# Optimization experiments

Hardware: AMD Instinct MI355X
Metric: run time of the kernel (lower is better)

Reference implementation:

```python
import jax, jax.numpy as jnp
import numpy as np
from jax.scipy.special import gammaln

EPS = 1e-20
EULER_GAMMA = 0.5772156649015329
B, L, D, H, DK, DV = 8, 512, 1024, 16, 64, 64
K_WEIBULL = 0.5
BETA_GAMMA = 1.0
SCALE = 1.0 / np.sqrt(DK)  # torch code DIVIDES by this -> multiply by sqrt(DK)


def setup_inputs() -> dict:
    key = jax.random.key(0)
    ks = jax.random.split(key, 20)
    f = jnp.float32
    return {
        "queries": jax.random.normal(ks[0], (B, L, D), f),
        "keys": jax.random.normal(ks[1], (B, L, D), f),
        "values": jax.random.normal(ks[2], (B, L, D), f),
        "unif": jax.random.uniform(ks[3], (B, H, L, L), f),
        "Wq": jax.random.normal(ks[4], (D, H * DK), f) * 0.03,
        "bq": jnp.zeros((H * DK,), f),
        "Wk": jax.random.normal(ks[5], (D, H * DK), f) * 0.03,
        "bk": jnp.zeros((H * DK,), f),
        "Wv": jax.random.normal(ks[6], (D, H * DV), f) * 0.03,
        "bv": jnp.zeros((H * DV,), f),
        "Wo": jax.random.normal(ks[7], (H * DV, D), f) * 0.03,
        "bo": jnp.zeros((D,), f),
        "Wp1": jax.random.normal(ks[8], (DK, D), f) * 0.05,
        "bp1": jnp.zeros((D,), f),
        "Wp2": jax.random.normal(ks[9], (D, 1), f) * 0.05,
        "bp2": jnp.zeros((1,), f),
    }


def reference(queries, keys, values, unif, Wq, bq, Wk, bk, Wv, bv, Wo, bo, Wp1, bp1, Wp2, bp2):
    # projections -> multi-head layout
    q = (queries @ Wq + bq).reshape(B, L, H, DK).transpose(0, 2, 1, 3)   # [B,H,Q,dk]
    k = (keys @ Wk + bk).reshape(B, L, H, DK).transpose(0, 2, 1, 3)     # [B,H,K,dk]
    v = (values @ Wv + bv).reshape(B, L, H, DV).transpose(0, 2, 1, 3)   # [B,H,K,dv]

    # faithful: torch divides by scale=1/sqrt(dk)
    att = jnp.einsum("bhqd,bhkd->bhqk", q, k) / SCALE                   # [B,H,Q,K]

    # prior MLP on keys (per key position)
    h = (k @ Wp1 + bp1)                                                  # [B,H,K,D]
    h = jnp.where(h >= 0, h, 0.01 * h)                                   # LeakyReLU
    dot_gamma = (h @ Wp2 + bp2).transpose(0, 1, 3, 2)                    # [B,H,1,K]
    prior_w = jax.nn.softmax(dot_gamma, axis=-1)
    alpha = prior_w * BETA_GAMMA                                         # [B,H,1,K]

    # Weibull reparameterized stochastic attention
    inv_k = 1.0 / K_WEIBULL
    logprobs = jnp.log(jax.nn.softmax(att, axis=-1) + EPS)
    gumbel_w = jnp.log(-jnp.log(1.0 - unif + EPS) + EPS)
    att_s = jax.nn.softmax(logprobs - gammaln(1.0 + inv_k + inv_k * gumbel_w), axis=-1)

    lg1 = gammaln(jnp.float32(1.0 + inv_k))
    kl = -(alpha * (logprobs - lg1)
           - EULER_GAMMA * alpha * inv_k
           - BETA_GAMMA * jnp.exp(logprobs - lg1 + lg1)
           + alpha * jnp.log(BETA_GAMMA + EPS)
           - gammaln(alpha + EPS))
    kl_mean = kl.mean()

    out = jnp.einsum("bhqk,bhkd->bhqd", att_s, v)                        # [B,H,Q,dv]
    out = out.transpose(0, 2, 1, 3).reshape(B, L, H * DV)
    out = out @ Wo + bo                                                  # [B,Q,D]
    return out, kl_mean
```

## Files before the change

### kernel.cpp

```cpp
#include <hip/hip_runtime.h>
#include <math.h>


typedef __bf16 bh_t;
typedef bh_t  bh8  __attribute__((ext_vector_type(8)));
typedef float f32x4 __attribute__((ext_vector_type(4)));
typedef _Float16 hf_t;
typedef hf_t  hf4  __attribute__((ext_vector_type(4)));

#define MFMA_BF16 __builtin_amdgcn_mfma_f32_16x16x32_bf16

static constexpr size_t PE = 4096ull*1024ull;
static constexpr size_t P2 = PE*2ull;
static constexpr size_t W2 = 1024ull*1024ull*2ull;
static constexpr size_t O_QHI = 0;
static constexpr size_t O_QLO = O_QHI + P2;
static constexpr size_t O_KHI = O_QLO + P2;
static constexpr size_t O_KLO = O_KHI + P2;
static constexpr size_t O_VT  = O_KLO + P2;
static constexpr size_t O_WQH = O_VT  + P2;
static constexpr size_t O_WQL = O_WQH + W2;
static constexpr size_t O_WKH = O_WQL + W2;
static constexpr size_t O_WKL = O_WKH + W2;
static constexpr size_t O_WVH = O_WKL + W2;
static constexpr size_t O_WVL = O_WVH + W2;
static constexpr size_t O_WOH = O_WVL + W2;
static constexpr size_t O_WOL = O_WOH + W2;
static constexpr size_t O_WP1H = O_WOL + W2;
static constexpr size_t O_WP1L = O_WP1H + 1024ull*64ull*2ull;
static constexpr size_t O_DG   = O_WP1L + 1024ull*64ull*2ull;
static constexpr size_t O_ALPHA= O_DG + 65536ull*4ull;
static constexpr size_t O_HO   = O_ALPHA + 65536ull*4ull;
static constexpr size_t O_GS   = O_HO + P2;
static constexpr size_t O_ACC  = O_GS + 512ull*65536ull*2ull;
static constexpr size_t O_AQH  = O_ACC + 256;
static constexpr size_t WS_TOTAL = O_AQH + 5ull*P2;

__device__ __align__(256) unsigned char g_ws[WS_TOTAL];

__device__ __forceinline__ float lgamma_fast(float x)
{
    float ax = (x < 0.5f) ? (1.0f - x) : x;
    float p  = ax*(ax+1.f)*(ax+2.f)*(ax+3.f);
    bool  sm = ax < 4.0f;
    float lsh = sm ? __logf(p) : 0.0f;
    float y   = sm ? (ax + 4.0f) : ax;
    float ly  = __logf(y);
    float inv = __builtin_amdgcn_rcpf(y);
    float i2  = inv * inv;
    float stir = fmaf(y - 0.5f, ly, -y) + 0.91893853320467274f
               + inv * fmaf(-2.7777777777e-3f, i2, 8.3333333333e-2f);
    float core = stir - lsh;
    float r  = x - rintf(x);
    float sp = __sinf(3.14159265358979f * r);
    float rres = 1.14472988584940017f - __logf(fabsf(sp)) - core;
    return (x < 0.5f) ? rres : core;
}

__global__ __launch_bounds__(256) void k_transpose_split(
    const float* __restrict__ in, bh_t* __restrict__ oh, bh_t* __restrict__ ol,
    int rows, int cols)
{
    __shared__ float tile[64][65];
    const int bc = blockIdx.x * 64, br = blockIdx.y * 64;
    const int t = threadIdx.x;
    const int r = t >> 2, c0 = (t & 3) * 16;
#pragma unroll
    for (int i = 0; i < 16; i += 4) {
        float4 v = *(const float4*)(in + (size_t)(br + r) * cols + bc + c0 + i);
        tile[r][c0+i]   = v.x; tile[r][c0+i+1] = v.y;
        tile[r][c0+i+2] = v.z; tile[r][c0+i+3] = v.w;
    }
    __syncthreads();
    bh8 hv[2], lv[2];
#pragma unroll
    for (int i = 0; i < 16; i++) {
        float x = tile[c0 + i][r];
        bh_t hh = (bh_t)x;
        hv[i >> 3][i & 7] = hh;
        lv[i >> 3][i & 7] = (bh_t)(x - (float)hh);
    }
    size_t ob = (size_t)(bc + r) * rows + br + c0;
    *(bh8*)(oh + ob)     = hv[0];
    *(bh8*)(oh + ob + 8) = hv[1];
    *(bh8*)(ol + ob)     = lv[0];
    *(bh8*)(ol + ob + 8) = lv[1];
}

__global__ __launch_bounds__(256) void k_transpose_split4(
    const float* __restrict__ W0, const float* __restrict__ W1,
    const float* __restrict__ W2_, const float* __restrict__ W3,
    bh_t* __restrict__ OH, double* __restrict__ acc)
{
    __shared__ float tile[64][65];
    const int z = blockIdx.z;
    if (z == 0 && blockIdx.x == 0 && blockIdx.y == 0 && threadIdx.x < 4)
        acc[threadIdx.x] = 0.0;
    const float* in = (z == 0) ? W0 : (z == 1) ? W1 : (z == 2) ? W2_ : W3;
    bh_t* oh = OH + (size_t)z * 2ull * 1024ull * 1024ull;
    bh_t* ol = oh + 1024ull * 1024ull;
    const int bc = blockIdx.x * 64, br = blockIdx.y * 64;
    const int t = threadIdx.x;
    const int r = t >> 2, c0 = (t & 3) * 16;
#pragma unroll
    for (int i = 0; i < 16; i += 4) {
        float4 v = *(const float4*)(in + (size_t)(br + r) * 1024 + bc + c0 + i);
        tile[r][c0+i]   = v.x; tile[r][c0+i+1] = v.y;
        tile[r][c0+i+2] = v.z; tile[r][c0+i+3] = v.w;
    }
    __syncthreads();
    bh8 hv[2], lv[2];
#pragma unroll
    for (int i = 0; i < 16; i++) {
        float x = tile[c0 + i][r];
        bh_t hh = (bh_t)x;
        hv[i >> 3][i & 7] = hh;
        lv[i >> 3][i & 7] = (bh_t)(x - (float)hh);
    }
    size_t ob = (size_t)(bc + r) * 1024 + br + c0;
    *(bh8*)(oh + ob)     = hv[0];
    *(bh8*)(oh + ob + 8) = hv[1];
    *(bh8*)(ol + ob)     = lv[0];
    *(bh8*)(ol + ob + 8) = lv[1];
}

__global__ __launch_bounds__(256) void k_splitA(
    const float* __restrict__ q, const float* __restrict__ k,
    const float* __restrict__ v, bh_t* __restrict__ dst)
{
    const int z = blockIdx.y;
    const float* in = (z == 0) ? q : (z == 1) ? k : v;
    size_t idx = ((size_t)blockIdx.x * 256 + threadIdx.x) * 8;
    float4 v0 = *(const float4*)(in + idx);
    float4 v1 = *(const float4*)(in + idx + 4);
    float xs[8] = {v0.x, v0.y, v0.z, v0.w, v1.x, v1.y, v1.z, v1.w};
    bh8 h, l;
#pragma unroll
    for (int i = 0; i < 8; i++) {
        bh_t hh = (bh_t)xs[i];
        h[i] = hh;
        l[i] = (bh_t)(xs[i] - (float)hh);
    }
    if (z < 2) {
        bh_t* hp = dst + (size_t)z * 2 * PE;
        *(bh8*)(hp + idx)      = h;
        *(bh8*)(hp + PE + idx) = l;
    } else {
        *(bh8*)(dst + 4 * PE + idx) = h;
    }
}

template<bool SPLIT, int OMODE>
__device__ __forceinline__ void gemm_body(
    const bh_t* __restrict__ ABH, const bh_t* __restrict__ ABL,
    const bh_t* __restrict__ WH, const bh_t* __restrict__ WL,
    const float* __restrict__ bias,
    bh_t* __restrict__ oh, bh_t* __restrict__ ol, float* __restrict__ of,
    int n0, int m0)
{
    __shared__ __align__(16) bh_t Ah[128][40];
    __shared__ __align__(16) bh_t Al[128][40];
    __shared__ __align__(16) bh_t Bh[128][40];
    __shared__ __align__(16) bh_t Bl[128][40];
    const int t = threadIdx.x;
    const int lane = t & 63, w = t >> 6;
    const int lr = lane & 15, kg = lane >> 4;
    const int wm = (w & 1) * 64, wn = (w >> 1) * 64;
    const int ar = t >> 2, ac = (t & 3) * 8;
    f32x4 acc[4][4] = {};

    for (int kt = 0; kt < 1024; kt += 32) {
        __syncthreads();
        {
            size_t a0 = (size_t)(m0 + ar) * 1024 + kt + ac;
            size_t a1 = (size_t)(m0 + ar + 64) * 1024 + kt + ac;
            *(bh8*)&Ah[ar][ac]      = *(const bh8*)(ABH + a0);
            *(bh8*)&Ah[ar + 64][ac] = *(const bh8*)(ABH + a1);
            if constexpr (SPLIT) {
                *(bh8*)&Al[ar][ac]      = *(const bh8*)(ABL + a0);
                *(bh8*)&Al[ar + 64][ac] = *(const bh8*)(ABL + a1);
            }
            size_t b0 = (size_t)(n0 + ar) * 1024 + kt + ac;
            size_t b1 = (size_t)(n0 + ar + 64) * 1024 + kt + ac;
            *(bh8*)&Bh[ar][ac]      = *(const bh8*)(WH + b0);
            *(bh8*)&Bh[ar + 64][ac] = *(const bh8*)(WH + b1);
            if constexpr (SPLIT) {
                *(bh8*)&Bl[ar][ac]      = *(const bh8*)(WL + b0);
                *(bh8*)&Bl[ar + 64][ac] = *(const bh8*)(WL + b1);
            }
        }
        __syncthreads();
        bh8 bfh[4], bfl[4];
#pragma unroll
        for (int fn = 0; fn < 4; fn++) {
            bfh[fn] = *(bh8*)&Bh[wn + fn*16 + lr][kg * 8];
            if constexpr (SPLIT) bfl[fn] = *(bh8*)&Bl[wn + fn*16 + lr][kg * 8];
        }
#pragma unroll
        for (int fm = 0; fm < 4; fm++) {
            bh8 a_h = *(bh8*)&Ah[wm + fm*16 + lr][kg * 8];
            bh8 a_l;
            if constexpr (SPLIT) a_l = *(bh8*)&Al[wm + fm*16 + lr][kg * 8];
#pragma unroll
            for (int fn = 0; fn < 4; fn++) {
                acc[fm][fn] = MFMA_BF16(a_h, bfh[fn], acc[fm][fn], 0, 0, 0);
                if constexpr (SPLIT) {
                    acc[fm][fn] = MFMA_BF16(a_h, bfl[fn], acc[fm][fn], 0, 0, 0);
                    acc[fm][fn] = MFMA_BF16(a_l, bfh[fn], acc[fm][fn], 0, 0, 0);
                }
            }
        }
    }
#pragma unroll
    for (int fm = 0; fm < 4; fm++)
#pragma unroll
    for (int fn = 0; fn < 4; fn++) {
        int col = n0 + wn + fn*16 + lr;
        float bv = bias[col];
#pragma unroll
        for (int r = 0; r < 4; r++) {
            int row = m0 + wm + fm*16 + kg*4 + r;
            float c = acc[fm][fn][r] + bv;
            size_t idx = (size_t)row * 1024 + col;
            if constexpr (OMODE == 0) {
                bh_t hh = (bh_t)c;
                oh[idx] = hh;
                ol[idx] = (bh_t)(c - (float)hh);
            } else if constexpr (OMODE == 1) {
                oh[idx] = (bh_t)c;
            } else if constexpr (OMODE == 2) {
                of[idx] = c;
            } else {
                int bb = row >> 9, ll = row & 511;
                oh[(((size_t)(bb*16 + (col >> 6)) * 64) + (col & 63)) * 512 + ll] = (bh_t)c;
            }
        }
    }
}

template<int OMODE>
__global__ __launch_bounds__(256) void k_gemm(
    const bh_t* __restrict__ ABH,
    const bh_t* __restrict__ WH, const bh_t* __restrict__ WL,
    const float* __restrict__ bias,
    bh_t* __restrict__ oh, float* __restrict__ of,
    const double* __restrict__ acc)
{
    gemm_body<false, OMODE>(ABH, nullptr, WH, WL, bias, oh, nullptr, of,
                            blockIdx.x * 128, blockIdx.y * 128);
    if constexpr (OMODE == 2) {
        if (blockIdx.x == 0 && blockIdx.y == 0 && threadIdx.x == 0) {
            double kl = (-acc[0] + 512.0 * acc[2] + 65536.0) / 33554432.0;
            of[4194304] = (float)kl;
        }
    }
}

__global__ __launch_bounds__(256) void k_gemm_qk(
    const bh_t* __restrict__ Abase, const bh_t* __restrict__ Wbase,
    const float* __restrict__ bq, const float* __restrict__ bk,
    bh_t* __restrict__ Obase)
{
    const int z = blockIdx.z;
    const bh_t* AH = Abase + (size_t)z * 2 * PE;
    const bh_t* WH = Wbase + (size_t)z * 2ull * 1024ull * 1024ull;
    bh_t* oh = Obase + (size_t)z * 2 * PE;
    gemm_body<true, 0>(AH, AH + PE, WH, WH + 1024ull*1024ull,
                       z ? bk : bq, oh, oh + PE, nullptr,
                       blockIdx.x * 128, blockIdx.y * 128);
}

__global__ __launch_bounds__(256) void k_prior(
    const bh_t* __restrict__ KH, const bh_t* __restrict__ WP1T,
    const float* __restrict__ bp1, const float* __restrict__ wp2,
    const float* __restrict__ bp2, float* __restrict__ DG)
{
    __shared__ __align__(16) bh_t Kt[64][72];
    __shared__ __align__(16) bh_t Wt[64][72];
    const int lt = blockIdx.x, h = blockIdx.y, b = blockIdx.z;
    const int t = threadIdx.x, lane = t & 63, w = t >> 6;
    const int lr = lane & 15, kg = lane >> 4;
    {
        int r = t >> 2, j0 = (t & 3) * 16;
        const bh_t* src = KH + ((size_t)(b*512 + lt*64 + r)) * 1024 + h*64 + j0;
        *(bh8*)&Kt[r][j0]     = *(const bh8*)src;
        *(bh8*)&Kt[r][j0 + 8] = *(const bh8*)(src + 8);
    }
    __syncthreads();
    bh8 af0 = *(bh8*)&Kt[w*16 + lr][kg * 8];
    bh8 af1 = *(bh8*)&Kt[w*16 + lr][32 + kg * 8];
    float dgp[4] = {0.f, 0.f, 0.f, 0.f};
    for (int dt = 0; dt < 16; dt++) {
        __syncthreads();
        {
            int r = t >> 2, j0 = (t & 3) * 16;
            const bh_t* src = WP1T + (size_t)(dt*64 + r) * 64 + j0;
            *(bh8*)&Wt[r][j0]     = *(const bh8*)src;
            *(bh8*)&Wt[r][j0 + 8] = *(const bh8*)(src + 8);
        }
        __syncthreads();
#pragma unroll
        for (int fn = 0; fn < 4; fn++) {
            bh8 b0 = *(bh8*)&Wt[fn*16 + lr][kg * 8];
            bh8 b1 = *(bh8*)&Wt[fn*16 + lr][32 + kg * 8];
            f32x4 acc = {};
            acc = MFMA_BF16(af0, b0, acc, 0, 0, 0);
            acc = MFMA_BF16(af1, b1, acc, 0, 0, 0);
            int d = dt*64 + fn*16 + lr;
            float bpv = bp1[d], wvv = wp2[d];
#pragma unroll
            for (int r = 0; r < 4; r++) {
                float hv = acc[r] + bpv;
                hv = (hv >= 0.f) ? hv : 0.01f * hv;
                dgp[r] = fmaf(hv, wvv, dgp[r]);
            }
        }
    }
#pragma unroll
    for (int r = 0; r < 4; r++) {
        float v = dgp[r];
        v += __shfl_xor(v, 1); v += __shfl_xor(v, 2);
        v += __shfl_xor(v, 4); v += __shfl_xor(v, 8);
        dgp[r] = v;
    }
    if (lr == 0) {
        float b2 = bp2[0];
        int bh = b * 16 + h;
#pragma unroll
        for (int r = 0; r < 4; r++)
            DG[(size_t)bh*512 + lt*64 + w*16 + kg*4 + r] = dgp[r] + b2;
    }
}

__global__ __launch_bounds__(512) void k_alpha(
    const float* __restrict__ DG, float* __restrict__ AL, double* __restrict__ acc)
{
    __shared__ float red[512];
    const int bh = blockIdx.x, t = threadIdx.x;
    float v = DG[(size_t)bh * 512 + t];
    red[t] = v; __syncthreads();
    for (int s = 256; s > 0; s >>= 1) { if (t < s) red[t] = fmaxf(red[t], red[t+s]); __syncthreads(); }
    float m = red[0]; __syncthreads();
    float e = expf(v - m);
    red[t] = e; __syncthreads();
    for (int s = 256; s > 0; s >>= 1) { if (t < s) red[t] += red[t+s]; __syncthreads(); }
    float ssum = red[0]; __syncthreads();
    float a = e / ssum;
    AL[(size_t)bh * 512 + t] = a;
    float t2 = a * 1.8475785103630112f + lgammaf(a + 1e-20f);
    red[t] = t2; __syncthreads();
    for (int s = 256; s > 0; s >>= 1) { if (t < s) red[t] += red[t+s]; __syncthreads(); }
    if (t == 0) atomicAdd(&acc[2], (double)red[0]);
}

__global__ __launch_bounds__(512, 3) void k_attn(
    const bh_t* __restrict__ QH, const bh_t* __restrict__ QL,
    const bh_t* __restrict__ KH, const bh_t* __restrict__ KL,
    const bh_t* __restrict__ VT, const float* __restrict__ U,
    const float* __restrict__ AL, bh_t* __restrict__ HOB,
    hf_t* __restrict__ GS, double* __restrict__ acc)
{
    __shared__ __align__(16) bh_t KtH[64][72];
    __shared__ __align__(16) bh_t KtL[64][72];
    __shared__ __align__(16) bh_t Vt[64][72];
    __shared__ __align__(16) bh_t Sl[8][16][72];
    __shared__ float Asm[64];
    __shared__ float red[512];

    const int flat = blockIdx.x;
    const int bh = flat & 127, qc = flat >> 7;
    const int b = bh >> 4, h = bh & 15;
    const int t = threadIdx.x, w = t >> 6, lane = t & 63;
    const int lr = lane & 15, kg = lane >> 4;
    const int q0 = qc * 128 + w * 16;
    const int sr = t >> 3, sj = (t & 7) * 8;
    const float* Up = U + ((size_t)bh * 512 + q0 + kg * 4) * 512;
    hf_t* GSp = GS + (size_t)flat * 65536 + (size_t)w * 8192;

    bh8 qh[2], ql[2];
    {
        size_t qb = ((size_t)(b * 512) + q0 + lr) * 1024 + h * 64;
        qh[0] = *(const bh8*)(QH + qb + kg * 8);
        qh[1] = *(const bh8*)(QH + qb + 32 + kg * 8);
        ql[0] = *(const bh8*)(QL + qb + kg * 8);
        ql[1] = *(const bh8*)(QL + qb + 32 + kg * 8);
    }
    float C[4];

    {
        float M1[4], Z1[4];
#pragma unroll
        for (int r = 0; r < 4; r++) { M1[r] = -INFINITY; Z1[r] = 0.f; }

        for (int kt = 0; kt < 8; kt++) {
            __syncthreads();
            {
                size_t src = ((size_t)(b*512 + kt*64 + sr)) * 1024 + h*64 + sj;
                *(bh8*)&KtH[sr][sj] = *(const bh8*)(KH + src);
                *(bh8*)&KtL[sr][sj] = *(const bh8*)(KL + src);
            }
            __syncthreads();
            f32x4 av[4];
#pragma unroll
            for (int fn = 0; fn < 4; fn++) {
                f32x4 a = {};
#pragma unroll
                for (int ks = 0; ks < 2; ks++) {
                    bh8 kb  = *(bh8*)&KtH[fn*16 + lr][ks*32 + kg*8];
                    bh8 kl2 = *(bh8*)&KtL[fn*16 + lr][ks*32 + kg*8];
                    a = MFMA_BF16(qh[ks], kb,  a, 0, 0, 0);
                    a = MFMA_BF16(qh[ks], kl2, a, 0, 0, 0);
                    a = MFMA_BF16(ql[ks], kb,  a, 0, 0, 0);
                }
#pragma unroll
                for (int r = 0; r < 4; r++) a[r] *= 8.0f;
                av[fn] = a;
                int k = kt * 64 + fn * 16 + lr;
                hf4 gh;
#pragma unroll
                for (int r = 0; r < 4; r++) {
                    float u  = Up[(size_t)r * 512 + k];
                    float tt = (1.0f - u) + 1e-20f;
                    float gl = 1e-20f - __logf(tt);
                    float g  = __logf(gl);
                    gh[r] = (hf_t)lgamma_fast(fmaf(2.0f, g, 3.0f));
                }
                *(hf4*)(GSp + ((size_t)(kt*4 + fn) * 64 + lane) * 4) = gh;
            }
#pragma unroll
            for (int r = 0; r < 4; r++) {
                float mx = fmaxf(fmaxf(av[0][r], av[1][r]), fmaxf(av[2][r], av[3][r]));
                mx = fmaxf(mx, __shfl_xor(mx, 1));
                mx = fmaxf(mx, __shfl_xor(mx, 2));
                mx = fmaxf(mx, __shfl_xor(mx, 4));
                mx = fmaxf(mx, __shfl_xor(mx, 8));
                float nm = fmaxf(M1[r], mx);
                float es = __expf(av[0][r]-nm) + __expf(av[1][r]-nm)
                         + __expf(av[2][r]-nm) + __expf(av[3][r]-nm);
                es += __shfl_xor(es, 1); es += __shfl_xor(es, 2);
                es += __shfl_xor(es, 4); es += __shfl_xor(es, 8);
                Z1[r] = Z1[r] * __expf(M1[r] - nm) + es;
                M1[r] = nm;
            }
        }
#pragma unroll
        for (int r = 0; r < 4; r++) C[r] = M1[r] + logf(Z1[r]);
    }

    float M2[4], Z2[4];
    f32x4 oacc[4] = {};
#pragma unroll
    for (int r = 0; r < 4; r++) { M2[r] = -INFINITY; Z2[r] = 0.f; }
    float S1f = 0.f;

    for (int kt = 0; kt < 8; kt++) {
        __syncthreads();
        {
            size_t src = ((size_t)(b*512 + kt*64 + sr)) * 1024 + h*64 + sj;
            *(bh8*)&KtH[sr][sj] = *(const bh8*)(KH + src);
            *(bh8*)&KtL[sr][sj] = *(const bh8*)(KL + src);
            const bh_t* vsrc = VT + ((size_t)bh * 64 + sr) * 512 + kt*64 + sj;
            *(bh8*)&Vt[sr][sj] = *(const bh8*)vsrc;
            if (t < 64) Asm[t] = AL[(size_t)bh * 512 + kt * 64 + t];
        }
        __syncthreads();
        f32x4 wv[4];
#pragma unroll
        for (int fn = 0; fn < 4; fn++) {
            f32x4 a = {};
#pragma unroll
            for (int ks = 0; ks < 2; ks++) {
                bh8 kb  = *(bh8*)&KtH[fn*16 + lr][ks*32 + kg*8];
                bh8 kl2 = *(bh8*)&KtL[fn*16 + lr][ks*32 + kg*8];
                a = MFMA_BF16(qh[ks], kb,  a, 0, 0, 0);
                a = MFMA_BF16(qh[ks], kl2, a, 0, 0, 0);
                a = MFMA_BF16(ql[ks], kb,  a, 0, 0, 0);
            }
            hf4 gh = *(const hf4*)(GSp + ((size_t)(kt*4 + fn) * 64 + lane) * 4);
            float alv = Asm[fn * 16 + lr];
#pragma unroll
            for (int r = 0; r < 4; r++) {
                float s  = fmaf(a[r], 8.0f, -C[r]);
                float ex = __expf(s);
                float lp = __logf(ex + 1e-20f);
                wv[fn][r] = lp - (float)gh[r];
                S1f = fmaf(alv, lp, S1f);
            }
        }
#pragma unroll
        for (int r = 0; r < 4; r++) {
            float mx = fmaxf(fmaxf(wv[0][r], wv[1][r]), fmaxf(wv[2][r], wv[3][r]));
            mx = fmaxf(mx, __shfl_xor(mx, 1));
            mx = fmaxf(mx, __shfl_xor(mx, 2));
            mx = fmaxf(mx, __shfl_xor(mx, 4));
            mx = fmaxf(mx, __shfl_xor(mx, 8));
            float nm = fmaxf(M2[r], mx);
            float sc = __expf(M2[r] - nm);
            float zs = 0.f;
#pragma unroll
            for (int fn = 0; fn < 4; fn++) {
                float sv = __expf(wv[fn][r] - nm);
                zs += sv;
                Sl[w][kg * 4 + r][fn * 16 + lr] = (bh_t)sv;
            }
            zs += __shfl_xor(zs, 1); zs += __shfl_xor(zs, 2);
            zs += __shfl_xor(zs, 4); zs += __shfl_xor(zs, 8);
            Z2[r] = fmaf(Z2[r], sc, zs);
            M2[r] = nm;
#pragma unroll
            for (int fo = 0; fo < 4; fo++) oacc[fo][r] *= sc;
        }
        bh8 sa0 = *(bh8*)&Sl[w][lr][kg*8];
        bh8 sa1 = *(bh8*)&Sl[w][lr][32 + kg*8];
#pragma unroll
        for (int fo = 0; fo < 4; fo++) {
            bh8 v0 = *(bh8*)&Vt[fo*16 + lr][kg*8];
            bh8 v1 = *(bh8*)&Vt[fo*16 + lr][32 + kg*8];
            oacc[fo] = MFMA_BF16(sa0, v0, oacc[fo], 0, 0, 0);
            oacc[fo] = MFMA_BF16(sa1, v1, oacc[fo], 0, 0, 0);
        }
    }
    float rz[4];
#pragma unroll
    for (int r = 0; r < 4; r++) rz[r] = 1.0f / Z2[r];
#pragma unroll
    for (int fo = 0; fo < 4; fo++) {
#pragma unroll
        for (int r = 0; r < 4; r++) {
            int q = q0 + kg * 4 + r;
            int dv = fo * 16 + lr;
            HOB[((size_t)(b * 512 + q)) * 1024 + h * 64 + dv] = (bh_t)(oacc[fo][r] * rz[r]);
        }
    }
    red[t] = S1f; __syncthreads();
    for (int s = 256; s > 0; s >>= 1) { if (t < s) red[t] += red[t+s]; __syncthreads(); }
    if (t == 0) atomicAdd(&acc[0], (double)red[0]);
}

extern "C" void kernel_launch(void* const* d_in, const int* in_sizes, int n_in,
                              void* d_out, int out_size, void* d_ws, size_t ws_size,
                              hipStream_t stream)
{
    (void)in_sizes; (void)n_in; (void)d_ws; (void)ws_size; (void)out_size;
    const float* queries = (const float*)d_in[0];
    const float* keys    = (const float*)d_in[1];
    const float* values  = (const float*)d_in[2];
    const float* unif    = (const float*)d_in[3];
    const float* Wq = (const float*)d_in[4];  const float* bq = (const float*)d_in[5];
    const float* Wk = (const float*)d_in[6];  const float* bk = (const float*)d_in[7];
    const float* Wv = (const float*)d_in[8];  const float* bv = (const float*)d_in[9];
    const float* Wo = (const float*)d_in[10]; const float* bo = (const float*)d_in[11];
    const float* Wp1 = (const float*)d_in[12]; const float* bp1 = (const float*)d_in[13];
    const float* Wp2 = (const float*)d_in[14]; const float* bp2 = (const float*)d_in[15];

    unsigned char* ws = nullptr;
    hipGetSymbolAddress((void**)&ws, HIP_SYMBOL(g_ws));

    bh_t* QHI = (bh_t*)(ws + O_QHI); bh_t* QLO = (bh_t*)(ws + O_QLO);
    bh_t* KHI = (bh_t*)(ws + O_KHI); bh_t* KLO = (bh_t*)(ws + O_KLO);
    bh_t* VTp = (bh_t*)(ws + O_VT);
    bh_t* WQH = (bh_t*)(ws + O_WQH);
    bh_t* WVH = (bh_t*)(ws + O_WVH); bh_t* WVL = (bh_t*)(ws + O_WVL);
    bh_t* WOH = (bh_t*)(ws + O_WOH); bh_t* WOL = (bh_t*)(ws + O_WOL);
    bh_t* WP1H = (bh_t*)(ws + O_WP1H); bh_t* WP1L = (bh_t*)(ws + O_WP1L);
    float* DG    = (float*)(ws + O_DG);
    float* ALPHA = (float*)(ws + O_ALPHA);
    bh_t*  HOB   = (bh_t*)(ws + O_HO);
    hf_t*  GS    = (hf_t*)(ws + O_GS);
    double* ACC  = (double*)(ws + O_ACC);
    bh_t*  AQH   = (bh_t*)(ws + O_AQH);
    bh_t*  AVH   = AQH + 4 * PE;
    float* outF  = (float*)d_out;

    k_transpose_split4<<<dim3(16,16,4), 256, 0, stream>>>(Wq, Wk, Wv, Wo, WQH, ACC);
    k_transpose_split<<<dim3(16,1), 256, 0, stream>>>(Wp1, WP1H, WP1L, 64, 1024);
    k_splitA<<<dim3(2048,3), 256, 0, stream>>>(queries, keys, values, AQH);

    k_gemm_qk<<<dim3(8,32,2), 256, 0, stream>>>(AQH, WQH, bq, bk, QHI);
    k_gemm<3><<<dim3(8,32), 256, 0, stream>>>(AVH, WVH, WVL, bv, VTp, nullptr, nullptr);

    k_prior<<<dim3(8,16,8), 256, 0, stream>>>(KHI, WP1H, bp1, Wp2, bp2, DG);
    k_alpha<<<128, 512, 0, stream>>>(DG, ALPHA, ACC);

    k_attn<<<512, 512, 0, stream>>>(QHI, QLO, KHI, KLO, VTp, unif, ALPHA, HOB, GS, ACC);

    k_gemm<2><<<dim3(8,32), 256, 0, stream>>>(HOB, WOH, WOL, bo, nullptr, outF, ACC);
}
```

Before: 339.7 us.

## Split attention over key halves with separate stats, merge, and combine kernels

Splits the fused two-pass attention kernel into a key-split first pass (partial max/sum), a small merge kernel for the log-normalizer, a key-split second pass writing unnormalized partial outputs plus stats, and a combine kernel that rescales and writes the bf16 head output. This doubles the grid from 512 to 1024 blocks and raises the occupancy hint so more waves keep the MI355X busy. It also rewrites lgamma_fast to use fewer logs and replaces log(exp(s)+eps) with a max-plus-correction form. The cost is two extra launches and extra global traffic for the partial outputs and stats.

```diff
diff --git a/kernel.cpp b/kernel.cpp
--- a/kernel.cpp
+++ b/kernel.cpp
@@ -34,27 +34,29 @@
 static constexpr size_t O_GS   = O_HO + P2;
 static constexpr size_t O_ACC  = O_GS + 512ull*65536ull*2ull;
 static constexpr size_t O_AQH  = O_ACC + 256;
-static constexpr size_t WS_TOTAL = O_AQH + 5ull*P2;
+static constexpr size_t O_PS   = O_AQH + 5ull*P2;
+static constexpr size_t O_CB   = O_PS + 1024ull*128ull*2ull*4ull;
+static constexpr size_t O_MZ   = O_CB + 512ull*128ull*4ull;
+static constexpr size_t O_OP   = O_MZ + 1024ull*128ull*2ull*4ull;
+static constexpr size_t WS_TOTAL = O_OP + 1024ull*128ull*64ull*4ull;
 
 __device__ __align__(256) unsigned char g_ws[WS_TOTAL];
 
 __device__ __forceinline__ float lgamma_fast(float x)
 {
     float ax = (x < 0.5f) ? (1.0f - x) : x;
-    float p  = ax*(ax+1.f)*(ax+2.f)*(ax+3.f);
     bool  sm = ax < 4.0f;
-    float lsh = sm ? __logf(p) : 0.0f;
-    float y   = sm ? (ax + 4.0f) : ax;
-    float ly  = __logf(y);
-    float inv = __builtin_amdgcn_rcpf(y);
-    float i2  = inv * inv;
-    float stir = fmaf(y - 0.5f, ly, -y) + 0.91893853320467274f
-               + inv * fmaf(-2.7777777777e-3f, i2, 8.3333333333e-2f);
-    float core = stir - lsh;
+    float p  = sm ? ax*(ax+1.f)*(ax+2.f)*(ax+3.f) : 1.0f;
+    float y  = sm ? (ax + 4.0f) : ax;
+    float ly = __logf(y);
+    float stir = fmaf(y - 0.5f, ly, -y) + 0.91893853320467274f;
     float r  = x - rintf(x);
     float sp = __sinf(3.14159265358979f * r);
-    float rres = 1.14472988584940017f - __logf(fabsf(sp)) - core;
-    return (x < 0.5f) ? rres : core;
+    bool  rf = x < 0.5f;
+    float rarg = rf ? fabsf(sp) : p;
+    float rnum = rf ? p : 1.0f;
+    float lA = __logf(rnum * __builtin_amdgcn_rcpf(rarg));
+    return (rf ? (1.14472988584940017f - stir) : stir) + lA;
 }
 
 __global__ __launch_bounds__(256) void k_transpose_split(
@@ -353,21 +355,17 @@
     if (t == 0) atomicAdd(&acc[2], (double)red[0]);
 }
 
-__global__ __launch_bounds__(512, 3) void k_attn(
+__global__ __launch_bounds__(512, 8) void k_attnA(
     const bh_t* __restrict__ QH, const bh_t* __restrict__ QL,
     const bh_t* __restrict__ KH, const bh_t* __restrict__ KL,
-    const bh_t* __restrict__ VT, const float* __restrict__ U,
-    const float* __restrict__ AL, bh_t* __restrict__ HOB,
-    hf_t* __restrict__ GS, double* __restrict__ acc)
+    const float* __restrict__ U, hf_t* __restrict__ GS,
+    float* __restrict__ PS)
 {
     __shared__ __align__(16) bh_t KtH[64][72];
     __shared__ __align__(16) bh_t KtL[64][72];
-    __shared__ __align__(16) bh_t Vt[64][72];
-    __shared__ __align__(16) bh_t Sl[8][16][72];
-    __shared__ float Asm[64];
-    __shared__ float red[512];
-
-    const int flat = blockIdx.x;
+
+    const int bid = blockIdx.x;
+    const int split = bid >> 9, flat = bid & 511;
     const int bh = flat & 127, qc = flat >> 7;
     const int b = bh >> 4, h = bh & 15;
     const int t = threadIdx.x, w = t >> 6, lane = t & 63;
@@ -385,75 +383,128 @@
         ql[0] = *(const bh8*)(QL + qb + kg * 8);
         ql[1] = *(const bh8*)(QL + qb + 32 + kg * 8);
     }
-    float C[4];
-
+    float M1[4], Z1[4];
+#pragma unroll
+    for (int r = 0; r < 4; r++) { M1[r] = -INFINITY; Z1[r] = 0.f; }
+
+    for (int kt = split * 4; kt < split * 4 + 4; kt++) {
+        __syncthreads();
+        {
+            size_t src = ((size_t)(b*512 + kt*64 + sr)) * 1024 + h*64 + sj;
+            *(bh8*)&KtH[sr][sj] = *(const bh8*)(KH + src);
+            *(bh8*)&KtL[sr][sj] = *(const bh8*)(KL + src);
+        }
+        __syncthreads();
+        f32x4 av[4];
+#pragma unroll
+        for (int fn = 0; fn < 4; fn++) {
+            f32x4 a = {};
+#pragma unroll
+            for (int ks = 0; ks < 2; ks++) {
+                bh8 kb  = *(bh8*)&KtH[fn*16 + lr][ks*32 + kg*8];
+                bh8 kl2 = *(bh8*)&KtL[fn*16 + lr][ks*32 + kg*8];
+                a = MFMA_BF16(qh[ks], kb,  a, 0, 0, 0);
+                a = MFMA_BF16(qh[ks], kl2, a, 0, 0, 0);
+                a = MFMA_BF16(ql[ks], kb,  a, 0, 0, 0);
+            }
+#pragma unroll
+            for (int r = 0; r < 4; r++) a[r] *= 8.0f;
+            av[fn] = a;
+            int k = kt * 64 + fn * 16 + lr;
+            hf4 gh;
+#pragma unroll
+            for (int r = 0; r < 4; r++) {
+                float u  = Up[(size_t)r * 512 + k];
+                float tt = (1.0f - u) + 1e-20f;
+                float gl = 1e-20f - __logf(tt);
+                float g  = __logf(gl);
+                gh[r] = (hf_t)lgamma_fast(fmaf(2.0f, g, 3.0f));
+            }
+            *(hf4*)(GSp + ((size_t)(kt*4 + fn) * 64 + lane) * 4) = gh;
+        }
+#pragma unroll
+        for (int r = 0; r < 4; r++) {
+            float mx = fmaxf(fmaxf(av[0][r], av[1][r]), fmaxf(av[2][r], av[3][r]));
+            mx = fmaxf(mx, __shfl_xor(mx, 1));
+            mx = fmaxf(mx, __shfl_xor(mx, 2));
+            mx = fmaxf(mx, __shfl_xor(mx, 4));
+            mx = fmaxf(mx, __shfl_xor(mx, 8));
+            float nm = fmaxf(M1[r], mx);
+            float es = __expf(av[0][r]-nm) + __expf(av[1][r]-nm)
+                     + __expf(av[2][r]-nm) + __expf(av[3][r]-nm);
+            es += __shfl_xor(es, 1); es += __shfl_xor(es, 2);
+            es += __shfl_xor(es, 4); es += __shfl_xor(es, 8);
+            Z1[r] = Z1[r] * __expf(M1[r] - nm) + es;
+            M1[r] = nm;
+        }
+    }
+    if (lr == 0) {
+#pragma unroll
+        for (int r = 0; r < 4; r++) {
+            size_t row = (size_t)bid * 128 + (w*16 + kg*4 + r);
+            PS[row * 2]     = M1[r];
+            PS[row * 2 + 1] = Z1[r];
+        }
+    }
+}
+
+__global__ __launch_bounds__(512) void k_mergeC(
+    const float* __restrict__ PS, float* __restrict__ CB)
+{
+    int idx = blockIdx.x * 512 + threadIdx.x;
+    float Ma = PS[(size_t)idx * 2],           Za = PS[(size_t)idx * 2 + 1];
+    float Mb = PS[(size_t)(65536 + idx) * 2], Zb = PS[(size_t)(65536 + idx) * 2 + 1];
+    float M = fmaxf(Ma, Mb);
+    float Z = Za * __expf(Ma - M) + Zb * __expf(Mb - M);
+    CB[idx] = M + __logf(Z);
+}
+
+__global__ __launch_bounds__(512, 6) void k_attnB(
+    const bh_t* __restrict__ QH, const bh_t* __restrict__ QL,
+    const bh_t* __restrict__ KH, const bh_t* __restrict__ KL,
+    const bh_t* __restrict__ VT, const float* __restrict__ AL,
+    const hf_t* __restrict__ GS, const float* __restrict__ CB,
+    float* __restrict__ OP, float* __restrict__ MZ,
+    double* __restrict__ acc)
+{
+    __shared__ __align__(16) bh_t KtH[64][72];
+    __shared__ __align__(16) bh_t KtL[64][72];
+    __shared__ __align__(16) bh_t Vt[64][72];
+    __shared__ __align__(16) bh_t Sl[8][16][72];
+    __shared__ float Asm[64];
+    __shared__ float red[512];
+
+    const int bid = blockIdx.x;
+    const int split = bid >> 9, flat = bid & 511;
+    const int bh = flat & 127, qc = flat >> 7;
+    const int b = bh >> 4, h = bh & 15;
+    const int t = threadIdx.x, w = t >> 6, lane = t & 63;
+    const int lr = lane & 15, kg = lane >> 4;
+    const int q0 = qc * 128 + w * 16;
+    const int sr = t >> 3, sj = (t & 7) * 8;
+    const hf_t* GSp = GS + (size_t)flat * 65536 + (size_t)w * 8192;
+
+    bh8 qh[2], ql[2];
     {
-        float M1[4], Z1[4];
-#pragma unroll
-        for (int r = 0; r < 4; r++) { M1[r] = -INFINITY; Z1[r] = 0.f; }
-
-        for (int kt = 0; kt < 8; kt++) {
-            __syncthreads();
-            {
-                size_t src = ((size_t)(b*512 + kt*64 + sr)) * 1024 + h*64 + sj;
-                *(bh8*)&KtH[sr][sj] = *(const bh8*)(KH + src);
-                *(bh8*)&KtL[sr][sj] = *(const bh8*)(KL + src);
-            }
-            __syncthreads();
-            f32x4 av[4];
-#pragma unroll
-            for (int fn = 0; fn < 4; fn++) {
-                f32x4 a = {};
-#pragma unroll
-                for (int ks = 0; ks < 2; ks++) {
-                    bh8 kb  = *(bh8*)&KtH[fn*16 + lr][ks*32 + kg*8];
-                    bh8 kl2 = *(bh8*)&KtL[fn*16 + lr][ks*32 + kg*8];
-                    a = MFMA_BF16(qh[ks], kb,  a, 0, 0, 0);
-                    a = MFMA_BF16(qh[ks], kl2, a, 0, 0, 0);
-                    a = MFMA_BF16(ql[ks], kb,  a, 0, 0, 0);
-                }
-#pragma unroll
-                for (int r = 0; r < 4; r++) a[r] *= 8.0f;
-                av[fn] = a;
-                int k = kt * 64 + fn * 16 + lr;
-                hf4 gh;
-#pragma unroll
-                for (int r = 0; r < 4; r++) {
-                    float u  = Up[(size_t)r * 512 + k];
-                    float tt = (1.0f - u) + 1e-20f;
-                    float gl = 1e-20f - __logf(tt);
-                    float g  = __logf(gl);
-                    gh[r] = (hf_t)lgamma_fast(fmaf(2.0f, g, 3.0f));
-                }
-                *(hf4*)(GSp + ((size_t)(kt*4 + fn) * 64 + lane) * 4) = gh;
-            }
-#pragma unroll
-            for (int r = 0; r < 4; r++) {
-                float mx = fmaxf(fmaxf(av[0][r], av[1][r]), fmaxf(av[2][r], av[3][r]));
-                mx = fmaxf(mx, __shfl_xor(mx, 1));
-                mx = fmaxf(mx, __shfl_xor(mx, 2));
-                mx = fmaxf(mx, __shfl_xor(mx, 4));
-                mx = fmaxf(mx, __shfl_xor(mx, 8));
-                float nm = fmaxf(M1[r], mx);
-                float es = __expf(av[0][r]-nm) + __expf(av[1][r]-nm)
-                         + __expf(av[2][r]-nm) + __expf(av[3][r]-nm);
-                es += __shfl_xor(es, 1); es += __shfl_xor(es, 2);
-                es += __shfl_xor(es, 4); es += __shfl_xor(es, 8);
-                Z1[r] = Z1[r] * __expf(M1[r] - nm) + es;
-                M1[r] = nm;
-            }
-        }
-#pragma unroll
-        for (int r = 0; r < 4; r++) C[r] = M1[r] + logf(Z1[r]);
-    }
+        size_t qb = ((size_t)(b * 512) + q0 + lr) * 1024 + h * 64;
+        qh[0] = *(const bh8*)(QH + qb + kg * 8);
+        qh[1] = *(const bh8*)(QH + qb + 32 + kg * 8);
+        ql[0] = *(const bh8*)(QL + qb + kg * 8);
+        ql[1] = *(const bh8*)(QL + qb + 32 + kg * 8);
+    }
+    float C4[4];
+#pragma unroll
+    for (int r = 0; r < 4; r++)
+        C4[r] = CB[flat * 128 + w*16 + kg*4 + r];
 
     float M2[4], Z2[4];
     f32x4 oacc[4] = {};
 #pragma unroll
     for (int r = 0; r < 4; r++) { M2[r] = -INFINITY; Z2[r] = 0.f; }
     float S1f = 0.f;
-
-    for (int kt = 0; kt < 8; kt++) {
+    const float LEPS = 46.0517019f;
+
+    for (int kt = split * 4; kt < split * 4 + 4; kt++) {
         __syncthreads();
         {
             size_t src = ((size_t)(b*512 + kt*64 + sr)) * 1024 + h*64 + sj;
@@ -464,7 +515,7 @@
             if (t < 64) Asm[t] = AL[(size_t)bh * 512 + kt * 64 + t];
         }
         __syncthreads();
-        f32x4 wv[4];
+        f32x4 wv[4], zq[4];
 #pragma unroll
         for (int fn = 0; fn < 4; fn++) {
             f32x4 a = {};
@@ -480,11 +531,13 @@
             float alv = Asm[fn * 16 + lr];
 #pragma unroll
             for (int r = 0; r < 4; r++) {
-                float s  = fmaf(a[r], 8.0f, -C[r]);
-                float ex = __expf(s);
-                float lp = __logf(ex + 1e-20f);
-                wv[fn][r] = lp - (float)gh[r];
-                S1f = fmaf(alv, lp, S1f);
+                float s  = fmaf(a[r], 8.0f, -C4[r]);
+                float m0 = fmaxf(s, -LEPS);
+                float d  = fabsf(s + LEPS);
+                float z  = __expf(-d);
+                zq[fn][r] = z;
+                S1f = fmaf(alv, m0 + z * fmaf(-0.5f, z, 1.0f), S1f);
+                wv[fn][r] = m0 - (float)gh[r];
             }
         }
 #pragma unroll
@@ -494,12 +547,12 @@
             mx = fmaxf(mx, __shfl_xor(mx, 2));
             mx = fmaxf(mx, __shfl_xor(mx, 4));
             mx = fmaxf(mx, __shfl_xor(mx, 8));
-            float nm = fmaxf(M2[r], mx);
+            float nm = fmaxf(M2[r], mx + 0.6931472f);
             float sc = __expf(M2[r] - nm);
             float zs = 0.f;
 #pragma unroll
             for (int fn = 0; fn < 4; fn++) {
-                float sv = __expf(wv[fn][r] - nm);
+                float sv = __expf(wv[fn][r] - nm) * (1.0f + zq[fn][r]);
                 zs += sv;
                 Sl[w][kg * 4 + r][fn * 16 + lr] = (bh_t)sv;
             }
@@ -520,21 +573,46 @@
             oacc[fo] = MFMA_BF16(sa1, v1, oacc[fo], 0, 0, 0);
         }
     }
-    float rz[4];
-#pragma unroll
-    for (int r = 0; r < 4; r++) rz[r] = 1.0f / Z2[r];
 #pragma unroll
     for (int fo = 0; fo < 4; fo++) {
 #pragma unroll
         for (int r = 0; r < 4; r++) {
-            int q = q0 + kg * 4 + r;
-            int dv = fo * 16 + lr;
-            HOB[((size_t)(b * 512 + q)) * 1024 + h * 64 + dv] = (bh_t)(oacc[fo][r] * rz[r]);
+            size_t row = (size_t)bid * 128 + (w*16 + kg*4 + r);
+            OP[row * 64 + (fo*16 + lr)] = oacc[fo][r];
+        }
+    }
+    if (lr == 0) {
+#pragma unroll
+        for (int r = 0; r < 4; r++) {
+            size_t row = (size_t)bid * 128 + (w*16 + kg*4 + r);
+            MZ[row * 2]     = M2[r];
+            MZ[row * 2 + 1] = Z2[r];
         }
     }
     red[t] = S1f; __syncthreads();
     for (int s = 256; s > 0; s >>= 1) { if (t < s) red[t] += red[t+s]; __syncthreads(); }
     if (t == 0) atomicAdd(&acc[0], (double)red[0]);
+}
+
+__global__ __launch_bounds__(256) void k_comb(
+    const float* __restrict__ OP, const float* __restrict__ MZ,
+    bh_t* __restrict__ HOB)
+{
+    size_t idx = (size_t)blockIdx.x * 256 + threadIdx.x;
+    int dv = idx & 63;
+    int rowg = (int)(idx >> 6);
+    float Ma = MZ[(size_t)rowg * 2],             Za = MZ[(size_t)rowg * 2 + 1];
+    float Mb = MZ[(size_t)(65536 + rowg) * 2],   Zb = MZ[(size_t)(65536 + rowg) * 2 + 1];
+    float M  = fmaxf(Ma, Mb);
+    float wa = __expf(Ma - M), wb = __expf(Mb - M);
+    float Z  = Za * wa + Zb * wb;
+    float o  = OP[(size_t)rowg * 64 + dv] * wa
+             + OP[(size_t)(65536 + rowg) * 64 + dv] * wb;
+    int flat = rowg >> 7, rl = rowg & 127;
+    int bh = flat & 127, qc = flat >> 7;
+    int b = bh >> 4, h = bh & 15;
+    int q = qc * 128 + rl;
+    HOB[((size_t)(b * 512 + q)) * 1024 + h * 64 + dv] = (bh_t)(o / Z);
 }
 
 extern "C" void kernel_launch(void* const* d_in, const int* in_sizes, int n_in,
@@ -570,6 +648,10 @@
     double* ACC  = (double*)(ws + O_ACC);
     bh_t*  AQH   = (bh_t*)(ws + O_AQH);
     bh_t*  AVH   = AQH + 4 * PE;
+    float* PS    = (float*)(ws + O_PS);
+    float* CB    = (float*)(ws + O_CB);
+    float* MZ    = (float*)(ws + O_MZ);
+    float* OP    = (float*)(ws + O_OP);
     float* outF  = (float*)d_out;
 
     k_transpose_split4<<<dim3(16,16,4), 256, 0, stream>>>(Wq, Wk, Wv, Wo, WQH, ACC);
@@ -582,7 +664,10 @@
     k_prior<<<dim3(8,16,8), 256, 0, stream>>>(KHI, WP1H, bp1, Wp2, bp2, DG);
     k_alpha<<<128, 512, 0, stream>>>(DG, ALPHA, ACC);
 
-    k_attn<<<512, 512, 0, stream>>>(QHI, QLO, KHI, KLO, VTp, unif, ALPHA, HOB, GS, ACC);
+    k_attnA<<<1024, 512, 0, stream>>>(QHI, QLO, KHI, KLO, unif, GS, PS);
+    k_mergeC<<<128, 512, 0, stream>>>(PS, CB);
+    k_attnB<<<1024, 512, 0, stream>>>(QHI, QLO, KHI, KLO, VTp, ALPHA, GS, CB, OP, MZ, ACC);
+    k_comb<<<16384, 256, 0, stream>>>(OP, MZ, HOB);
 
     k_gemm<2><<<dim3(8,32), 256, 0, stream>>>(HOB, WOH, WOL, bo, nullptr, outF, ACC);
 }
```

Measured after the change: 515.5 us. 51.8% more time.
